# Performance work log

Hardware: AMD Instinct MI355X
Metric: run time of the kernel (lower is better)

Reference implementation:

```python
import jax, jax.numpy as jnp
import numpy as np

ALPHA = 0.2      # LeakyReLU negative slope
NEG = -9e15     # mask fill value, as in pyGAT

B, N, NFEAT, NHID, NCLASS, NHEADS = 4, 2048, 128, 64, 32, 8


def setup_inputs() -> dict:
    key = jax.random.key(0)
    ks = jax.random.split(key, 8)
    x = jax.random.normal(ks[0], (B, N, NFEAT), dtype=jnp.float32)
    adj = jax.random.randint(ks[1], (B, N, N), 0, 2, dtype=jnp.int32)
    W = jax.random.normal(ks[2], (NHEADS, NFEAT, NHID), dtype=jnp.float32) * 0.1
    a1 = jax.random.normal(ks[3], (NHEADS, NHID), dtype=jnp.float32) * 0.1
    a2 = jax.random.normal(ks[4], (NHEADS, NHID), dtype=jnp.float32) * 0.1
    Wo = jax.random.normal(ks[5], (NHEADS * NHID, NCLASS), dtype=jnp.float32) * 0.1
    ao1 = jax.random.normal(ks[6], (NCLASS,), dtype=jnp.float32) * 0.1
    ao2 = jax.random.normal(ks[7], (NCLASS,), dtype=jnp.float32) * 0.1
    return {"x": x, "adj": adj, "W": W, "a1": a1, "a2": a2,
            "Wo": Wo, "ao1": ao1, "ao2": ao2}


def _gat_forward(x, adj, W, a1, a2, Wo, ao1, ao2):
    mask = adj > 0  # [B, N, N]
    # --- multi-head layer (concat=True) ---
    Wh = jnp.einsum('bnf,hfd->bhnd', x, W)          # [B,H,N,nhid]
    f1 = jnp.einsum('bhnd,hd->bhn', Wh, a1)          # Wh @ a[:nhid]
    f2 = jnp.einsum('bhnd,hd->bhn', Wh, a2)          # Wh @ a[nhid:]
    e = jax.nn.leaky_relu(f1[..., :, None] + f2[..., None, :], ALPHA)
    att = jax.nn.softmax(jnp.where(mask[:, None], e, NEG), axis=-1)
    h = jax.nn.elu(jnp.einsum('bhnm,bhmd->bhnd', att, Wh))  # [B,H,N,nhid]
    # torch.cat along dim=2: [B, N, H*nhid]
    h = jnp.transpose(h, (0, 2, 1, 3)).reshape(B, N, NHEADS * NHID)
    # (dropout layers are no-ops in eval mode)
    # --- output head (concat=False, no ELU) ---
    Wh2 = jnp.einsum('bnf,fc->bnc', h, Wo)           # [B,N,nclass]
    g1 = jnp.einsum('bnc,c->bn', Wh2, ao1)
    g2 = jnp.einsum('bnc,c->bn', Wh2, ao2)
    e2 = jax.nn.leaky_relu(g1[:, :, None] + g2[:, None, :], ALPHA)
    att2 = jax.nn.softmax(jnp.where(mask, e2, NEG), axis=-1)
    return jnp.einsum('bnm,bmc->bnc', att2, Wh2)     # [B,N,nclass]


def reference(x, adj, W, a1, a2, Wo, ao1, ao2):
    return _gat_forward(x, adj, W, a1, a2, Wo, ao1, ao2)
```

## Files before the change

kernel.cpp:

```cpp
#include <hip/hip_runtime.h>


typedef short  short8  __attribute__((ext_vector_type(8)));
typedef float  float4_ __attribute__((ext_vector_type(4)));
typedef float  float2_ __attribute__((ext_vector_type(2)));
typedef unsigned int uint4_ __attribute__((ext_vector_type(4)));

#if __has_builtin(__builtin_amdgcn_exp2f)
#define EXP2(x) __builtin_amdgcn_exp2f(x)
#else
#define EXP2(x) __expf((x) * 0.69314718055994531f)
#endif
#define LOG2E 1.44269504088896340f

static __device__ __forceinline__ unsigned short f2bf(float f) {
  unsigned u = __float_as_uint(f);
  u += 0x7fffu + ((u >> 16) & 1u);
  return (unsigned short)(u >> 16);
}
static __device__ __forceinline__ unsigned pk2bf(float a, float b) {
  return (unsigned)f2bf(a) | ((unsigned)f2bf(b) << 16);
}

static __device__ __forceinline__ unsigned bitm(unsigned mb, int jj) {
#if __has_builtin(__builtin_amdgcn_sbfe)
  return (unsigned)__builtin_amdgcn_sbfe((int)mb, jj, 1);
#else
  return 0u - ((mb >> jj) & 1u);
#endif
}

static __device__ __forceinline__ unsigned wpair(float2_ t, unsigned m0, unsigned m1) {
  float2_ l = __builtin_elementwise_max(t * 0.2f, t);
  unsigned e0 = __float_as_uint(EXP2(l.x)) & m0;
  unsigned e1 = __float_as_uint(EXP2(l.y)) & m1;
  return __builtin_amdgcn_perm(e1, e0, 0x07060302u);
}

__global__ __launch_bounds__(256) void k_wfrag(
    const float* __restrict__ Wm, short* __restrict__ Wf) {
  const int T = blockIdx.x * 256 + threadIdx.x;
  const int lane = T & 63;
  int r = T >> 6;
  const int nt = r & 3; r >>= 2;
  const int kstep = r & 3; r >>= 2;
  const int h = r;
  const int kk = kstep * 32 + (lane >> 4) * 8;
  const int n = nt * 16 + (lane & 15);
  const float* sp = Wm + h * 8192 + kk * 64 + n;
  short8 o;
  #pragma unroll
  for (int jj = 0; jj < 8; ++jj) o[jj] = (short)f2bf(sp[jj * 64]);
  *(short8*)(Wf + T * 8) = o;
}

__global__ __launch_bounds__(256) void k_front(
    const int* __restrict__ adj, unsigned long long* __restrict__ maskb,
    const float* __restrict__ x, const short* __restrict__ Wf,
    const float* __restrict__ a1, const float* __restrict__ a2,
    short* __restrict__ WhF, float* __restrict__ f1, float* __restrict__ f2) {
  __shared__ float wsm[64 * 68];
  const int bx = blockIdx.x;
  const int t = threadIdx.x;
  if (bx >= 1024) {
    const int lane = t & 63, wid = t >> 6;
    const int s = lane & 15;
    const long long row0 = (long long)(bx - 1024) * 4;
    for (int rr = 0; rr < 4; ++rr) {
      const long long row = row0 + rr;
      const int4* src = (const int4*)(adj + row * 2048);
      #pragma unroll
      for (int c = 0; c < 2; ++c) {
        int4 v = src[c * 256 + t];
        unsigned nib = (v.x != 0 ? 1u : 0u) | (v.y != 0 ? 2u : 0u) |
                       (v.z != 0 ? 4u : 0u) | (v.w != 0 ? 8u : 0u);
        unsigned lo = (s < 8) ? (nib << (s * 4)) : 0u;
        unsigned hi = (s >= 8) ? (nib << ((s - 8) * 4)) : 0u;
        #pragma unroll
        for (int off = 1; off < 16; off <<= 1) {
          lo |= __shfl_xor(lo, off);
          hi |= __shfl_xor(hi, off);
        }
        if (s == 0) {
          int word = c * 16 + wid * 4 + (lane >> 4);
          maskb[row * 32 + word] = ((unsigned long long)hi << 32) | (unsigned long long)lo;
        }
      }
    }
    return;
  }
  const int itile = bx & 31, bh = bx >> 5;
  const int b = bh >> 3, h = bh & 7;
  const int i0 = itile * 64;
  const int lane = t & 63, w = t >> 6;
  const int cl = lane & 15, q = lane >> 4;
  const float* xrow = x + ((long long)b * 2048 + i0 + w * 16 + cl) * 128;
  const short* wfh = Wf + h * 8192;
  float4_ acc0 = {0.f, 0.f, 0.f, 0.f}, acc1 = acc0, acc2 = acc0, acc3 = acc0;
  #pragma unroll
  for (int kstep = 0; kstep < 4; ++kstep) {
    const float* xp = xrow + kstep * 32 + q * 8;
    const float4 xa = *(const float4*)xp;
    const float4 xb = *(const float4*)(xp + 4);
    uint4_ ap;
    ap.x = pk2bf(xa.x, xa.y);
    ap.y = pk2bf(xa.z, xa.w);
    ap.z = pk2bf(xb.x, xb.y);
    ap.w = pk2bf(xb.z, xb.w);
    const short8 af = __builtin_bit_cast(short8, ap);
    const short* bp = wfh + kstep * 2048 + lane * 8;
    const short8 b0 = *(const short8*)(bp);
    const short8 b1 = *(const short8*)(bp + 512);
    const short8 b2 = *(const short8*)(bp + 1024);
    const short8 b3 = *(const short8*)(bp + 1536);
    acc0 = __builtin_amdgcn_mfma_f32_16x16x32_bf16(af, b0, acc0, 0, 0, 0);
    acc1 = __builtin_amdgcn_mfma_f32_16x16x32_bf16(af, b1, acc1, 0, 0, 0);
    acc2 = __builtin_amdgcn_mfma_f32_16x16x32_bf16(af, b2, acc2, 0, 0, 0);
    acc3 = __builtin_amdgcn_mfma_f32_16x16x32_bf16(af, b3, acc3, 0, 0, 0);
  }
  {
    float4_ accs[4] = {acc0, acc1, acc2, acc3};
    #pragma unroll
    for (int nt = 0; nt < 4; ++nt)
      #pragma unroll
      for (int reg = 0; reg < 4; ++reg)
        wsm[(w * 16 + q * 4 + reg) * 68 + nt * 16 + cl] = accs[nt][reg];
  }
  __syncthreads();
  {
    const int row = t >> 2, seg = t & 3;
    const float* wr = wsm + row * 68 + seg * 16;
    const float4* a1p = (const float4*)(a1 + h * 64 + seg * 16);
    const float4* a2p = (const float4*)(a2 + h * 64 + seg * 16);
    float p1 = 0.f, p2 = 0.f;
    #pragma unroll
    for (int u = 0; u < 4; ++u) {
      const float4 wv = *(const float4*)(wr + u * 4);
      const float4 v1 = a1p[u];
      const float4 v2 = a2p[u];
      p1 += wv.x * v1.x + wv.y * v1.y + wv.z * v1.z + wv.w * v1.w;
      p2 += wv.x * v2.x + wv.y * v2.y + wv.z * v2.z + wv.w * v2.w;
    }
    p1 += __shfl_xor(p1, 1); p1 += __shfl_xor(p1, 2);
    p2 += __shfl_xor(p2, 1); p2 += __shfl_xor(p2, 2);
    if (seg == 0) {
      f1[(long long)bh * 2048 + i0 + row] = p1 * LOG2E;
      f2[(long long)bh * 2048 + i0 + row] = p2 * LOG2E;
    }
  }
  #pragma unroll
  for (int u = 0; u < 2; ++u) {
    const int idx = u * 256 + t;
    const int l2 = idx & 63, nt2 = (idx >> 6) & 3, ks2 = idx >> 8;
    const int jrow = ks2 * 32 + (l2 >> 4) * 8;
    const int d = nt2 * 16 + (l2 & 15);
    short8 o;
    #pragma unroll
    for (int jj = 0; jj < 8; ++jj) o[jj] = (short)f2bf(wsm[(jrow + jj) * 68 + d]);
    const long long off = (long long)bh * 131072 + (long long)itile * 4096 +
                          ks2 * 2048 + nt2 * 512 + l2 * 8;
    *(short8*)(WhF + off) = o;
  }
}

__global__ __launch_bounds__(256) void k_attn1(
    const short* __restrict__ whf, const float* __restrict__ f1v,
    const float* __restrict__ f2v, const unsigned long long* __restrict__ maskb,
    float* __restrict__ h1) {
  __shared__ short bsm[2][8192];
  __shared__ float f2s[2048];
  const int bh = blockIdx.y, b = bh >> 3, hh = bh & 7;
  const int t = threadIdx.x;
  const int lane = t & 63, wid = t >> 6;
  const int cl = lane & 15, q = lane >> 4;
  const long long i_g = (long long)blockIdx.x * 64 + wid * 16 + cl;
  const float f1i = f1v[(long long)bh * 2048 + i_g];
  const float2_ f1i2 = {f1i, f1i};
  const uint2* mpp = (const uint2*)(maskb + ((long long)b * 2048 + i_g) * 32);
  const float* f2b = f2v + (long long)bh * 2048;
  const short* whfb = whf + (long long)bh * 131072;
  const float4* gB = (const float4*)whfb;
  const short8 vones = {16256, 16256, 16256, 16256, 16256, 16256, 16256, 16256};
  ((float4*)f2s)[t] = ((const float4*)f2b)[t];
  ((float4*)f2s)[256 + t] = ((const float4*)f2b)[256 + t];
  {
    float4 st0[4];
    #pragma unroll
    for (int u = 0; u < 4; ++u) st0[u] = gB[u * 256 + t];
    #pragma unroll
    for (int u = 0; u < 4; ++u) ((float4*)bsm[0])[u * 256 + t] = st0[u];
  }
  uint2 mw0_c = mpp[0], mw1_c = mpp[1];
  float4_ acc0 = {0.f, 0.f, 0.f, 0.f}, acc1 = acc0, acc2 = acc0, acc3 = acc0;
  float4_ accz = acc0;
  const int qs = q * 8;
  for (int s = 0; s < 16; ++s) {
    float4 stn0, stn1, stn2, stn3;
    if (s < 15) {
      const float4* gp = gB + (s + 1) * 1024 + t;
      stn0 = gp[0]; stn1 = gp[256]; stn2 = gp[512]; stn3 = gp[768];
    }
    const uint2 mwA = mw0_c, mwB = mw1_c;
    if (s < 15) { mw0_c = mpp[s * 2 + 2]; mw1_c = mpp[s * 2 + 3]; }
    __syncthreads();
    const short* bsb = bsm[s & 1] + lane * 8;
    #pragma unroll
    for (int jc2 = 0; jc2 < 2; ++jc2) {
      const int jc = s * 2 + jc2;
      const uint2 mw = jc2 ? mwB : mwA;
      #pragma unroll
      for (int ks = 0; ks < 2; ++ks) {
        const unsigned mb = (ks ? mw.y : mw.x) >> qs;
        const float* fp = f2s + jc * 64 + ks * 32 + qs;
        const float4 fa = *(const float4*)fp;
        const float4 fb = *(const float4*)(fp + 4);
        uint4_ pk;
        pk.x = wpair(f1i2 + (float2_){fa.x, fa.y}, bitm(mb, 0), bitm(mb, 1));
        pk.y = wpair(f1i2 + (float2_){fa.z, fa.w}, bitm(mb, 2), bitm(mb, 3));
        pk.z = wpair(f1i2 + (float2_){fb.x, fb.y}, bitm(mb, 4), bitm(mb, 5));
        pk.w = wpair(f1i2 + (float2_){fb.z, fb.w}, bitm(mb, 6), bitm(mb, 7));
        const short8 af = __builtin_bit_cast(short8, pk);
        const short* bp = bsb + (jc2 * 2 + ks) * 2048;
        short8 b0 = *(const short8*)(bp);
        short8 b1 = *(const short8*)(bp + 512);
        short8 b2 = *(const short8*)(bp + 1024);
        short8 b3 = *(const short8*)(bp + 1536);
        acc0 = __builtin_amdgcn_mfma_f32_16x16x32_bf16(af, b0, acc0, 0, 0, 0);
        acc1 = __builtin_amdgcn_mfma_f32_16x16x32_bf16(af, b1, acc1, 0, 0, 0);
        acc2 = __builtin_amdgcn_mfma_f32_16x16x32_bf16(af, b2, acc2, 0, 0, 0);
        acc3 = __builtin_amdgcn_mfma_f32_16x16x32_bf16(af, b3, acc3, 0, 0, 0);
        accz = __builtin_amdgcn_mfma_f32_16x16x32_bf16(af, vones, accz, 0, 0, 0);
      }
    }
    if (s < 15) {
      float4* dp = (float4*)bsm[(s + 1) & 1] + t;
      dp[0] = stn0; dp[256] = stn1; dp[512] = stn2; dp[768] = stn3;
    }
  }
  float4_ accs[4] = {acc0, acc1, acc2, acc3};
  #pragma unroll
  for (int reg = 0; reg < 4; ++reg) {
    const int ir = q * 4 + reg;
    const float rz = 1.f / accz[reg];
    const long long row = (long long)blockIdx.x * 64 + wid * 16 + ir;
    float* op = h1 + ((long long)b * 2048 + row) * 512 + hh * 64 + cl;
    #pragma unroll
    for (int nt = 0; nt < 4; ++nt) {
      float v = accs[nt][reg] * rz;
      v = (v > 0.f) ? v : (__expf(v) - 1.f);
      op[nt * 16] = v;
    }
  }
}

__global__ __launch_bounds__(256) void k_ogemm(
    const float* __restrict__ h1, const float* __restrict__ Wo,
    const float* __restrict__ ao1, const float* __restrict__ ao2,
    short* __restrict__ Wh2F, float* __restrict__ g1, float* __restrict__ g2) {
  __shared__ float hsm[32 * 512];
  __shared__ float w2s[32 * 33];
  const long long r0 = (long long)blockIdx.x * 32;
  const int t = threadIdx.x;
  const int c = t & 31, ty = t >> 5;
  const float4* src = (const float4*)(h1 + r0 * 512);
  float4* dstv = (float4*)hsm;
  #pragma unroll
  for (int j = 0; j < 16; ++j) dstv[j * 256 + t] = src[j * 256 + t];
  __syncthreads();
  float acc0 = 0.f, acc1 = 0.f, acc2 = 0.f, acc3 = 0.f;
  for (int kc = 0; kc < 128; ++kc) {
    const int k = kc * 4;
    const float w0 = Wo[(k + 0) * 32 + c];
    const float w1 = Wo[(k + 1) * 32 + c];
    const float w2 = Wo[(k + 2) * 32 + c];
    const float w3 = Wo[(k + 3) * 32 + c];
    const float4 ha = *(const float4*)&hsm[(ty + 0) * 512 + k];
    const float4 hb = *(const float4*)&hsm[(ty + 8) * 512 + k];
    const float4 hc = *(const float4*)&hsm[(ty + 16) * 512 + k];
    const float4 hd = *(const float4*)&hsm[(ty + 24) * 512 + k];
    acc0 += ha.x * w0 + ha.y * w1 + ha.z * w2 + ha.w * w3;
    acc1 += hb.x * w0 + hb.y * w1 + hb.z * w2 + hb.w * w3;
    acc2 += hc.x * w0 + hc.y * w1 + hc.z * w2 + hc.w * w3;
    acc3 += hd.x * w0 + hd.y * w1 + hd.z * w2 + hd.w * w3;
  }
  const float a1c = ao1[c], a2c = ao2[c];
  const float accs[4] = {acc0, acc1, acc2, acc3};
  #pragma unroll
  for (int m = 0; m < 4; ++m) {
    const long long row = r0 + ty + 8 * m;
    w2s[(ty + 8 * m) * 33 + c] = accs[m];
    float p1 = accs[m] * a1c, p2 = accs[m] * a2c;
    #pragma unroll
    for (int off = 1; off < 32; off <<= 1) {
      p1 += __shfl_xor(p1, off);
      p2 += __shfl_xor(p2, off);
    }
    if (c == 0) { g1[row] = p1 * LOG2E; g2[row] = p2 * LOG2E; }
  }
  __syncthreads();
  if (t < 128) {
    const int l2 = t & 63, nt2 = t >> 6;
    const int g = blockIdx.x >> 6, jc = (blockIdx.x >> 1) & 31, ks2 = blockIdx.x & 1;
    const int lr = (l2 >> 4) * 8;
    const int d = nt2 * 16 + (l2 & 15);
    short8 o;
    #pragma unroll
    for (int jj = 0; jj < 8; ++jj) o[jj] = (short)f2bf(w2s[(lr + jj) * 33 + d]);
    const long long off = (long long)g * 65536 + jc * 2048 + ks2 * 1024 +
                          nt2 * 512 + l2 * 8;
    *(short8*)(Wh2F + off) = o;
  }
}

__global__ __launch_bounds__(256) void k_attn2(
    const short* __restrict__ whf2, const float* __restrict__ g1v,
    const float* __restrict__ g2v, const unsigned long long* __restrict__ maskb,
    float* __restrict__ outp) {
  __shared__ float accs[4][16][33];
  __shared__ float zsh[64];
  const int b = blockIdx.y;
  const long long i0 = (long long)blockIdx.x * 16;
  const int t = threadIdx.x, lane = t & 63, wid = t >> 6;
  const int cl = lane & 15, q = lane >> 4;
  const float g1i = g1v[(long long)b * 2048 + i0 + cl];
  const float2_ g1i2 = {g1i, g1i};
  const uint2* mpp = (const uint2*)(maskb + ((long long)b * 2048 + i0 + cl) * 32);
  const float* g2b = g2v + (long long)b * 2048;
  const short* wb = whf2 + (long long)b * 65536;
  const short8 vones = {16256, 16256, 16256, 16256, 16256, 16256, 16256, 16256};
  float4_ acc0 = {0.f, 0.f, 0.f, 0.f}, acc1 = acc0, accz = acc0;
  const int qs = q * 8;
  const int jc0 = wid * 8;
  uint2 mw_c = mpp[jc0];
  float4 fa0_c = *(const float4*)(g2b + jc0 * 64 + qs);
  float4 fb0_c = *(const float4*)(g2b + jc0 * 64 + qs + 4);
  float4 fa1_c = *(const float4*)(g2b + jc0 * 64 + 32 + qs);
  float4 fb1_c = *(const float4*)(g2b + jc0 * 64 + 36 + qs);
  for (int c8 = 0; c8 < 8; ++c8) {
    const int jc = jc0 + c8;
    const uint2 mw = mw_c;
    const float4 fa0 = fa0_c, fb0 = fb0_c, fa1 = fa1_c, fb1 = fb1_c;
    {
      const int jn = jc + ((c8 < 7) ? 1 : 0);
      const float* fp = g2b + jn * 64 + qs;
      mw_c = mpp[jn];
      fa0_c = *(const float4*)fp;
      fb0_c = *(const float4*)(fp + 4);
      fa1_c = *(const float4*)(fp + 32);
      fb1_c = *(const float4*)(fp + 36);
    }
    const short* bb = wb + (jc * 2) * 1024 + lane * 8;
    {
      const unsigned mb = mw.x >> qs;
      uint4_ pk;
      pk.x = wpair(g1i2 + (float2_){fa0.x, fa0.y}, bitm(mb, 0), bitm(mb, 1));
      pk.y = wpair(g1i2 + (float2_){fa0.z, fa0.w}, bitm(mb, 2), bitm(mb, 3));
      pk.z = wpair(g1i2 + (float2_){fb0.x, fb0.y}, bitm(mb, 4), bitm(mb, 5));
      pk.w = wpair(g1i2 + (float2_){fb0.z, fb0.w}, bitm(mb, 6), bitm(mb, 7));
      const short8 af = __builtin_bit_cast(short8, pk);
      short8 b0 = *(const short8*)bb;
      short8 b1 = *(const short8*)(bb + 512);
      acc0 = __builtin_amdgcn_mfma_f32_16x16x32_bf16(af, b0, acc0, 0, 0, 0);
      acc1 = __builtin_amdgcn_mfma_f32_16x16x32_bf16(af, b1, acc1, 0, 0, 0);
      accz = __builtin_amdgcn_mfma_f32_16x16x32_bf16(af, vones, accz, 0, 0, 0);
    }
    {
      const unsigned mb = mw.y >> qs;
      uint4_ pk;
      pk.x = wpair(g1i2 + (float2_){fa1.x, fa1.y}, bitm(mb, 0), bitm(mb, 1));
      pk.y = wpair(g1i2 + (float2_){fa1.z, fa1.w}, bitm(mb, 2), bitm(mb, 3));
      pk.z = wpair(g1i2 + (float2_){fb1.x, fb1.y}, bitm(mb, 4), bitm(mb, 5));
      pk.w = wpair(g1i2 + (float2_){fb1.z, fb1.w}, bitm(mb, 6), bitm(mb, 7));
      const short8 af = __builtin_bit_cast(short8, pk);
      const short* bk = bb + 1024;
      short8 b0 = *(const short8*)bk;
      short8 b1 = *(const short8*)(bk + 512);
      acc0 = __builtin_amdgcn_mfma_f32_16x16x32_bf16(af, b0, acc0, 0, 0, 0);
      acc1 = __builtin_amdgcn_mfma_f32_16x16x32_bf16(af, b1, acc1, 0, 0, 0);
      accz = __builtin_amdgcn_mfma_f32_16x16x32_bf16(af, vones, accz, 0, 0, 0);
    }
  }
  if (cl == 0) {
    #pragma unroll
    for (int reg = 0; reg < 4; ++reg) zsh[wid * 16 + q * 4 + reg] = accz[reg];
  }
  float4_ a01[2] = {acc0, acc1};
  #pragma unroll
  for (int nt = 0; nt < 2; ++nt)
    #pragma unroll
    for (int reg = 0; reg < 4; ++reg)
      accs[wid][q * 4 + reg][nt * 16 + cl] = a01[nt][reg];
  __syncthreads();
  #pragma unroll
  for (int r = 0; r < 2; ++r) {
    int o = r * 256 + t;
    int il = o >> 5, c = o & 31;
    float s = accs[0][il][c] + accs[1][il][c] + accs[2][il][c] + accs[3][il][c];
    float Z = zsh[il] + zsh[16 + il] + zsh[32 + il] + zsh[48 + il];
    outp[((long long)b * 2048 + i0 + il) * 32 + c] = s / Z;
  }
}

extern "C" void kernel_launch(void* const* d_in, const int* in_sizes, int n_in,
                              void* d_out, int out_size, void* d_ws, size_t ws_size,
                              hipStream_t stream) {
  const float* x   = (const float*)d_in[0];
  const int*   adj = (const int*)d_in[1];
  const float* W   = (const float*)d_in[2];
  const float* a1  = (const float*)d_in[3];
  const float* a2  = (const float*)d_in[4];
  const float* Wo  = (const float*)d_in[5];
  const float* ao1 = (const float*)d_in[6];
  const float* ao2 = (const float*)d_in[7];
  float* out = (float*)d_out;
  char* ws = (char*)d_ws;

  unsigned long long* maskb = (unsigned long long*)(ws + 0);
  short* Wf   = (short*)(ws + 2097152);
  short* WhF  = (short*)(ws + 18874368);
  float* f1   = (float*)(ws + 27262976);
  float* f2   = (float*)(ws + 27525120);
  float* h1   = (float*)(ws + 27787264);
  short* Wh2F = (short*)(ws + 45613056);
  float* g1   = (float*)(ws + 46137344);
  float* g2   = (float*)(ws + 46170112);

  hipLaunchKernelGGL(k_wfrag, dim3(32), dim3(256), 0, stream, W, Wf);
  hipLaunchKernelGGL(k_front, dim3(3072), dim3(256), 0, stream, adj, maskb,
                     x, Wf, a1, a2, WhF, f1, f2);
  hipLaunchKernelGGL(k_attn1, dim3(32, 32), dim3(256), 0, stream, WhF, f1, f2, maskb, h1);
  hipLaunchKernelGGL(k_ogemm, dim3(256), dim3(256), 0, stream, h1, Wo, ao1, ao2,
                     Wh2F, g1, g2);
  hipLaunchKernelGGL(k_attn2, dim3(128, 4), dim3(256), 0, stream, Wh2F, g1, g2, maskb, out);
}
```

Measured before the change: 190.6 us.

## Factor attention exponentials into per-row and per-column terms; MFMA output GEMM

The per-element exp2(leaky_relu(f1+f2)) is rewritten as max(exp2(f1)*exp2(f2), exp2(0.2f1)*exp2(0.2f2)). The per-column exponentials are precomputed once and packed as two bf16 values, so the inner attention loop does two multiplies and a max instead of exp2 calls. The first attention kernel now writes h in bf16 MFMA fragment layout, and the output GEMM becomes an MFMA kernel using a pre-fragmented Wo. Exp-based factorization can overflow or underflow for large logits, and bf16 rounding of the exponentials reduces accuracy.

```diff
diff --git a/kernel.cpp b/kernel.cpp
--- a/kernel.cpp
+++ b/kernel.cpp
@@ -21,6 +21,9 @@
 static __device__ __forceinline__ unsigned pk2bf(float a, float b) {
   return (unsigned)f2bf(a) | ((unsigned)f2bf(b) << 16);
 }
+static __device__ __forceinline__ unsigned upack(float s) {
+  return ((unsigned)f2bf(EXP2(0.2f * s)) << 16) | f2bf(EXP2(s));
+}
 
 static __device__ __forceinline__ unsigned bitm(unsigned mb, int jj) {
 #if __has_builtin(__builtin_amdgcn_sbfe)
@@ -30,35 +33,53 @@
 #endif
 }
 
-static __device__ __forceinline__ unsigned wpair(float2_ t, unsigned m0, unsigned m1) {
-  float2_ l = __builtin_elementwise_max(t * 0.2f, t);
-  unsigned e0 = __float_as_uint(EXP2(l.x)) & m0;
-  unsigned e1 = __float_as_uint(EXP2(l.y)) & m1;
+static __device__ __forceinline__ unsigned wmax2(unsigned w0, unsigned w1,
+    unsigned m0, unsigned m1, float2_ Av, float2_ A2v) {
+  float2_ lo = {__uint_as_float(w0 << 16), __uint_as_float(w1 << 16)};
+  float2_ hi = {__uint_as_float(w0 & 0xFFFF0000u), __uint_as_float(w1 & 0xFFFF0000u)};
+  float2_ p = Av * lo;
+  float2_ n = A2v * hi;
+  float2_ m = __builtin_elementwise_max(p, n);
+  unsigned e0 = __float_as_uint(m.x) & m0;
+  unsigned e1 = __float_as_uint(m.y) & m1;
   return __builtin_amdgcn_perm(e1, e0, 0x07060302u);
 }
 
 __global__ __launch_bounds__(256) void k_wfrag(
-    const float* __restrict__ Wm, short* __restrict__ Wf) {
-  const int T = blockIdx.x * 256 + threadIdx.x;
-  const int lane = T & 63;
-  int r = T >> 6;
-  const int nt = r & 3; r >>= 2;
-  const int kstep = r & 3; r >>= 2;
-  const int h = r;
-  const int kk = kstep * 32 + (lane >> 4) * 8;
-  const int n = nt * 16 + (lane & 15);
-  const float* sp = Wm + h * 8192 + kk * 64 + n;
-  short8 o;
-  #pragma unroll
-  for (int jj = 0; jj < 8; ++jj) o[jj] = (short)f2bf(sp[jj * 64]);
-  *(short8*)(Wf + T * 8) = o;
+    const float* __restrict__ Wm, const float* __restrict__ Wo,
+    short* __restrict__ Wf, short* __restrict__ WoF) {
+  if (blockIdx.x < 32) {
+    const int T = blockIdx.x * 256 + threadIdx.x;
+    const int lane = T & 63;
+    int r = T >> 6;
+    const int nt = r & 3; r >>= 2;
+    const int kstep = r & 3; r >>= 2;
+    const int h = r;
+    const int kk = kstep * 32 + (lane >> 4) * 8;
+    const int n = nt * 16 + (lane & 15);
+    const float* sp = Wm + h * 8192 + kk * 64 + n;
+    short8 o;
+    #pragma unroll
+    for (int jj = 0; jj < 8; ++jj) o[jj] = (short)f2bf(sp[jj * 64]);
+    *(short8*)(Wf + T * 8) = o;
+  } else {
+    const int T = (blockIdx.x - 32) * 256 + threadIdx.x;
+    const int lane = T & 63;
+    const int nt = (T >> 6) & 1, kstep = T >> 7;
+    const int kk = kstep * 32 + (lane >> 4) * 8;
+    const int n = nt * 16 + (lane & 15);
+    short8 o;
+    #pragma unroll
+    for (int jj = 0; jj < 8; ++jj) o[jj] = (short)f2bf(Wo[(kk + jj) * 32 + n]);
+    *(short8*)(WoF + T * 8) = o;
+  }
 }
 
 __global__ __launch_bounds__(256) void k_front(
     const int* __restrict__ adj, unsigned long long* __restrict__ maskb,
     const float* __restrict__ x, const short* __restrict__ Wf,
     const float* __restrict__ a1, const float* __restrict__ a2,
-    short* __restrict__ WhF, float* __restrict__ f1, float* __restrict__ f2) {
+    short* __restrict__ WhF, float* __restrict__ f1, unsigned* __restrict__ f2p) {
   __shared__ float wsm[64 * 68];
   const int bx = blockIdx.x;
   const int t = threadIdx.x;
@@ -145,7 +166,7 @@
     p2 += __shfl_xor(p2, 1); p2 += __shfl_xor(p2, 2);
     if (seg == 0) {
       f1[(long long)bh * 2048 + i0 + row] = p1 * LOG2E;
-      f2[(long long)bh * 2048 + i0 + row] = p2 * LOG2E;
+      f2p[(long long)bh * 2048 + i0 + row] = upack(p2 * LOG2E);
     }
   }
   #pragma unroll
@@ -165,24 +186,25 @@
 
 __global__ __launch_bounds__(256) void k_attn1(
     const short* __restrict__ whf, const float* __restrict__ f1v,
-    const float* __restrict__ f2v, const unsigned long long* __restrict__ maskb,
-    float* __restrict__ h1) {
+    const unsigned* __restrict__ f2pv, const unsigned long long* __restrict__ maskb,
+    short* __restrict__ hA) {
   __shared__ short bsm[2][8192];
-  __shared__ float f2s[2048];
+  __shared__ unsigned f2s[2048];
   const int bh = blockIdx.y, b = bh >> 3, hh = bh & 7;
   const int t = threadIdx.x;
   const int lane = t & 63, wid = t >> 6;
   const int cl = lane & 15, q = lane >> 4;
   const long long i_g = (long long)blockIdx.x * 64 + wid * 16 + cl;
   const float f1i = f1v[(long long)bh * 2048 + i_g];
-  const float2_ f1i2 = {f1i, f1i};
+  const float A = EXP2(f1i), A2 = EXP2(0.2f * f1i);
+  const float2_ Av = {A, A}, A2v = {A2, A2};
   const uint2* mpp = (const uint2*)(maskb + ((long long)b * 2048 + i_g) * 32);
-  const float* f2b = f2v + (long long)bh * 2048;
+  const unsigned* f2b = f2pv + (long long)bh * 2048;
   const short* whfb = whf + (long long)bh * 131072;
   const float4* gB = (const float4*)whfb;
   const short8 vones = {16256, 16256, 16256, 16256, 16256, 16256, 16256, 16256};
-  ((float4*)f2s)[t] = ((const float4*)f2b)[t];
-  ((float4*)f2s)[256 + t] = ((const float4*)f2b)[256 + t];
+  ((uint4_*)f2s)[t] = ((const uint4_*)f2b)[t];
+  ((uint4_*)f2s)[256 + t] = ((const uint4_*)f2b)[256 + t];
   {
     float4 st0[4];
     #pragma unroll
@@ -211,14 +233,14 @@
       #pragma unroll
       for (int ks = 0; ks < 2; ++ks) {
         const unsigned mb = (ks ? mw.y : mw.x) >> qs;
-        const float* fp = f2s + jc * 64 + ks * 32 + qs;
-        const float4 fa = *(const float4*)fp;
-        const float4 fb = *(const float4*)(fp + 4);
+        const unsigned* up = f2s + jc * 64 + ks * 32 + qs;
+        const uint4_ wa = *(const uint4_*)up;
+        const uint4_ wb = *(const uint4_*)(up + 4);
         uint4_ pk;
-        pk.x = wpair(f1i2 + (float2_){fa.x, fa.y}, bitm(mb, 0), bitm(mb, 1));
-        pk.y = wpair(f1i2 + (float2_){fa.z, fa.w}, bitm(mb, 2), bitm(mb, 3));
-        pk.z = wpair(f1i2 + (float2_){fb.x, fb.y}, bitm(mb, 4), bitm(mb, 5));
-        pk.w = wpair(f1i2 + (float2_){fb.z, fb.w}, bitm(mb, 6), bitm(mb, 7));
+        pk.x = wmax2(wa.x, wa.y, bitm(mb, 0), bitm(mb, 1), Av, A2v);
+        pk.y = wmax2(wa.z, wa.w, bitm(mb, 2), bitm(mb, 3), Av, A2v);
+        pk.z = wmax2(wb.x, wb.y, bitm(mb, 4), bitm(mb, 5), Av, A2v);
+        pk.w = wmax2(wb.z, wb.w, bitm(mb, 6), bitm(mb, 7), Av, A2v);
         const short8 af = __builtin_bit_cast(short8, pk);
         const short* bp = bsb + (jc2 * 2 + ks) * 2048;
         short8 b0 = *(const short8*)(bp);
@@ -237,75 +259,87 @@
       dp[0] = stn0; dp[256] = stn1; dp[512] = stn2; dp[768] = stn3;
     }
   }
-  float4_ accs[4] = {acc0, acc1, acc2, acc3};
+  __syncthreads();
+  float* hs = (float*)bsm;
+  {
+    float4_ accs[4] = {acc0, acc1, acc2, acc3};
+    #pragma unroll
+    for (int reg = 0; reg < 4; ++reg) {
+      const float rz = 1.f / accz[reg];
+      #pragma unroll
+      for (int nt = 0; nt < 4; ++nt) {
+        float v = accs[nt][reg] * rz;
+        v = (v > 0.f) ? v : (__expf(v) - 1.f);
+        hs[(wid * 16 + q * 4 + reg) * 68 + nt * 16 + cl] = v;
+      }
+    }
+  }
+  __syncthreads();
+  const int rtg0 = b * 128 + blockIdx.x * 4;
+  #pragma unroll
+  for (int u = 0; u < 2; ++u) {
+    const int id = u * 256 + t;
+    const int l2 = id & 63, ks2 = (id >> 6) & 1, rtile = id >> 7;
+    const int rowl = rtile * 16 + (l2 & 15);
+    const int d = ks2 * 32 + (l2 >> 4) * 8;
+    const float* hp = hs + rowl * 68 + d;
+    const float4 va = *(const float4*)hp;
+    const float4 vb = *(const float4*)(hp + 4);
+    uint4_ o;
+    o.x = pk2bf(va.x, va.y); o.y = pk2bf(va.z, va.w);
+    o.z = pk2bf(vb.x, vb.y); o.w = pk2bf(vb.z, vb.w);
+    const long long rt = rtg0 + rtile;
+    const int kstep = hh * 2 + ks2;
+    *(uint4_*)(hA + ((rt * 16 + kstep) * 64 + l2) * 8) = o;
+  }
+}
+
+__global__ __launch_bounds__(128) void k_ogemm(
+    const short* __restrict__ hA, const short* __restrict__ WoF,
+    const float* __restrict__ ao1, const float* __restrict__ ao2,
+    short* __restrict__ Wh2F, float* __restrict__ g1, unsigned* __restrict__ g2p) {
+  __shared__ float w2s[32 * 36];
+  const int t = threadIdx.x, lane = t & 63, wv = t >> 6;
+  const int cl = lane & 15, q = lane >> 4;
+  const long long rt = (long long)blockIdx.x * 2 + wv;
+  float4_ acc0 = {0.f, 0.f, 0.f, 0.f}, acc1 = acc0;
+  const short* ap = hA + rt * 8192 + lane * 8;
+  const short* bp = WoF + lane * 8;
+  #pragma unroll
+  for (int kstep = 0; kstep < 16; ++kstep) {
+    const short8 af = *(const short8*)(ap + kstep * 512);
+    const short8 b0 = *(const short8*)(bp + kstep * 1024);
+    const short8 b1 = *(const short8*)(bp + kstep * 1024 + 512);
+    acc0 = __builtin_amdgcn_mfma_f32_16x16x32_bf16(af, b0, acc0, 0, 0, 0);
+    acc1 = __builtin_amdgcn_mfma_f32_16x16x32_bf16(af, b1, acc1, 0, 0, 0);
+  }
+  const float o1a = ao1[cl], o1b = ao1[cl + 16];
+  const float o2a = ao2[cl], o2b = ao2[cl + 16];
   #pragma unroll
   for (int reg = 0; reg < 4; ++reg) {
-    const int ir = q * 4 + reg;
-    const float rz = 1.f / accz[reg];
-    const long long row = (long long)blockIdx.x * 64 + wid * 16 + ir;
-    float* op = h1 + ((long long)b * 2048 + row) * 512 + hh * 64 + cl;
-    #pragma unroll
-    for (int nt = 0; nt < 4; ++nt) {
-      float v = accs[nt][reg] * rz;
-      v = (v > 0.f) ? v : (__expf(v) - 1.f);
-      op[nt * 16] = v;
-    }
-  }
-}
-
-__global__ __launch_bounds__(256) void k_ogemm(
-    const float* __restrict__ h1, const float* __restrict__ Wo,
-    const float* __restrict__ ao1, const float* __restrict__ ao2,
-    short* __restrict__ Wh2F, float* __restrict__ g1, float* __restrict__ g2) {
-  __shared__ float hsm[32 * 512];
-  __shared__ float w2s[32 * 33];
-  const long long r0 = (long long)blockIdx.x * 32;
-  const int t = threadIdx.x;
-  const int c = t & 31, ty = t >> 5;
-  const float4* src = (const float4*)(h1 + r0 * 512);
-  float4* dstv = (float4*)hsm;
-  #pragma unroll
-  for (int j = 0; j < 16; ++j) dstv[j * 256 + t] = src[j * 256 + t];
+    const int rowl = wv * 16 + q * 4 + reg;
+    w2s[rowl * 36 + cl] = acc0[reg];
+    w2s[rowl * 36 + 16 + cl] = acc1[reg];
+    float p1 = acc0[reg] * o1a + acc1[reg] * o1b;
+    float p2 = acc0[reg] * o2a + acc1[reg] * o2b;
+    p1 += __shfl_xor(p1, 1); p1 += __shfl_xor(p1, 2);
+    p1 += __shfl_xor(p1, 4); p1 += __shfl_xor(p1, 8);
+    p2 += __shfl_xor(p2, 1); p2 += __shfl_xor(p2, 2);
+    p2 += __shfl_xor(p2, 4); p2 += __shfl_xor(p2, 8);
+    if (cl == 0) {
+      const long long row = (long long)blockIdx.x * 32 + rowl;
+      g1[row] = p1 * LOG2E;
+      g2p[row] = upack(p2 * LOG2E);
+    }
+  }
   __syncthreads();
-  float acc0 = 0.f, acc1 = 0.f, acc2 = 0.f, acc3 = 0.f;
-  for (int kc = 0; kc < 128; ++kc) {
-    const int k = kc * 4;
-    const float w0 = Wo[(k + 0) * 32 + c];
-    const float w1 = Wo[(k + 1) * 32 + c];
-    const float w2 = Wo[(k + 2) * 32 + c];
-    const float w3 = Wo[(k + 3) * 32 + c];
-    const float4 ha = *(const float4*)&hsm[(ty + 0) * 512 + k];
-    const float4 hb = *(const float4*)&hsm[(ty + 8) * 512 + k];
-    const float4 hc = *(const float4*)&hsm[(ty + 16) * 512 + k];
-    const float4 hd = *(const float4*)&hsm[(ty + 24) * 512 + k];
-    acc0 += ha.x * w0 + ha.y * w1 + ha.z * w2 + ha.w * w3;
-    acc1 += hb.x * w0 + hb.y * w1 + hb.z * w2 + hb.w * w3;
-    acc2 += hc.x * w0 + hc.y * w1 + hc.z * w2 + hc.w * w3;
-    acc3 += hd.x * w0 + hd.y * w1 + hd.z * w2 + hd.w * w3;
-  }
-  const float a1c = ao1[c], a2c = ao2[c];
-  const float accs[4] = {acc0, acc1, acc2, acc3};
-  #pragma unroll
-  for (int m = 0; m < 4; ++m) {
-    const long long row = r0 + ty + 8 * m;
-    w2s[(ty + 8 * m) * 33 + c] = accs[m];
-    float p1 = accs[m] * a1c, p2 = accs[m] * a2c;
-    #pragma unroll
-    for (int off = 1; off < 32; off <<= 1) {
-      p1 += __shfl_xor(p1, off);
-      p2 += __shfl_xor(p2, off);
-    }
-    if (c == 0) { g1[row] = p1 * LOG2E; g2[row] = p2 * LOG2E; }
-  }
-  __syncthreads();
-  if (t < 128) {
+  {
     const int l2 = t & 63, nt2 = t >> 6;
     const int g = blockIdx.x >> 6, jc = (blockIdx.x >> 1) & 31, ks2 = blockIdx.x & 1;
-    const int lr = (l2 >> 4) * 8;
-    const int d = nt2 * 16 + (l2 & 15);
+    const int kb = (l2 >> 4) * 8, n = nt2 * 16 + (l2 & 15);
     short8 o;
     #pragma unroll
-    for (int jj = 0; jj < 8; ++jj) o[jj] = (short)f2bf(w2s[(lr + jj) * 33 + d]);
+    for (int jj = 0; jj < 8; ++jj) o[jj] = (short)f2bf(w2s[(kb + jj) * 36 + n]);
     const long long off = (long long)g * 65536 + jc * 2048 + ks2 * 1024 +
                           nt2 * 512 + l2 * 8;
     *(short8*)(Wh2F + off) = o;
@@ -314,7 +348,7 @@
 
 __global__ __launch_bounds__(256) void k_attn2(
     const short* __restrict__ whf2, const float* __restrict__ g1v,
-    const float* __restrict__ g2v, const unsigned long long* __restrict__ maskb,
+    const unsigned* __restrict__ g2pv, const unsigned long long* __restrict__ maskb,
     float* __restrict__ outp) {
   __shared__ float accs[4][16][33];
   __shared__ float zsh[64];
@@ -323,40 +357,41 @@
   const int t = threadIdx.x, lane = t & 63, wid = t >> 6;
   const int cl = lane & 15, q = lane >> 4;
   const float g1i = g1v[(long long)b * 2048 + i0 + cl];
-  const float2_ g1i2 = {g1i, g1i};
+  const float A = EXP2(g1i), A2 = EXP2(0.2f * g1i);
+  const float2_ Av = {A, A}, A2v = {A2, A2};
   const uint2* mpp = (const uint2*)(maskb + ((long long)b * 2048 + i0 + cl) * 32);
-  const float* g2b = g2v + (long long)b * 2048;
+  const unsigned* g2b = g2pv + (long long)b * 2048;
   const short* wb = whf2 + (long long)b * 65536;
   const short8 vones = {16256, 16256, 16256, 16256, 16256, 16256, 16256, 16256};
   float4_ acc0 = {0.f, 0.f, 0.f, 0.f}, acc1 = acc0, accz = acc0;
   const int qs = q * 8;
   const int jc0 = wid * 8;
   uint2 mw_c = mpp[jc0];
-  float4 fa0_c = *(const float4*)(g2b + jc0 * 64 + qs);
-  float4 fb0_c = *(const float4*)(g2b + jc0 * 64 + qs + 4);
-  float4 fa1_c = *(const float4*)(g2b + jc0 * 64 + 32 + qs);
-  float4 fb1_c = *(const float4*)(g2b + jc0 * 64 + 36 + qs);
+  uint4_ wa0_c = *(const uint4_*)(g2b + jc0 * 64 + qs);
+  uint4_ wb0_c = *(const uint4_*)(g2b + jc0 * 64 + qs + 4);
+  uint4_ wa1_c = *(const uint4_*)(g2b + jc0 * 64 + 32 + qs);
+  uint4_ wb1_c = *(const uint4_*)(g2b + jc0 * 64 + 36 + qs);
   for (int c8 = 0; c8 < 8; ++c8) {
     const int jc = jc0 + c8;
     const uint2 mw = mw_c;
-    const float4 fa0 = fa0_c, fb0 = fb0_c, fa1 = fa1_c, fb1 = fb1_c;
+    const uint4_ wa0 = wa0_c, wb0 = wb0_c, wa1 = wa1_c, wb1 = wb1_c;
     {
       const int jn = jc + ((c8 < 7) ? 1 : 0);
-      const float* fp = g2b + jn * 64 + qs;
+      const unsigned* fp = g2b + jn * 64 + qs;
       mw_c = mpp[jn];
-      fa0_c = *(const float4*)fp;
-      fb0_c = *(const float4*)(fp + 4);
-      fa1_c = *(const float4*)(fp + 32);
-      fb1_c = *(const float4*)(fp + 36);
+      wa0_c = *(const uint4_*)fp;
+      wb0_c = *(const uint4_*)(fp + 4);
+      wa1_c = *(const uint4_*)(fp + 32);
+      wb1_c = *(const uint4_*)(fp + 36);
     }
     const short* bb = wb + (jc * 2) * 1024 + lane * 8;
     {
       const unsigned mb = mw.x >> qs;
       uint4_ pk;
-      pk.x = wpair(g1i2 + (float2_){fa0.x, fa0.y}, bitm(mb, 0), bitm(mb, 1));
-      pk.y = wpair(g1i2 + (float2_){fa0.z, fa0.w}, bitm(mb, 2), bitm(mb, 3));
-      pk.z = wpair(g1i2 + (float2_){fb0.x, fb0.y}, bitm(mb, 4), bitm(mb, 5));
-      pk.w = wpair(g1i2 + (float2_){fb0.z, fb0.w}, bitm(mb, 6), bitm(mb, 7));
+      pk.x = wmax2(wa0.x, wa0.y, bitm(mb, 0), bitm(mb, 1), Av, A2v);
+      pk.y = wmax2(wa0.z, wa0.w, bitm(mb, 2), bitm(mb, 3), Av, A2v);
+      pk.z = wmax2(wb0.x, wb0.y, bitm(mb, 4), bitm(mb, 5), Av, A2v);
+      pk.w = wmax2(wb0.z, wb0.w, bitm(mb, 6), bitm(mb, 7), Av, A2v);
       const short8 af = __builtin_bit_cast(short8, pk);
       short8 b0 = *(const short8*)bb;
       short8 b1 = *(const short8*)(bb + 512);
@@ -367,10 +402,10 @@
     {
       const unsigned mb = mw.y >> qs;
       uint4_ pk;
-      pk.x = wpair(g1i2 + (float2_){fa1.x, fa1.y}, bitm(mb, 0), bitm(mb, 1));
-      pk.y = wpair(g1i2 + (float2_){fa1.z, fa1.w}, bitm(mb, 2), bitm(mb, 3));
-      pk.z = wpair(g1i2 + (float2_){fb1.x, fb1.y}, bitm(mb, 4), bitm(mb, 5));
-      pk.w = wpair(g1i2 + (float2_){fb1.z, fb1.w}, bitm(mb, 6), bitm(mb, 7));
+      pk.x = wmax2(wa1.x, wa1.y, bitm(mb, 0), bitm(mb, 1), Av, A2v);
+      pk.y = wmax2(wa1.z, wa1.w, bitm(mb, 2), bitm(mb, 3), Av, A2v);
+      pk.z = wmax2(wb1.x, wb1.y, bitm(mb, 4), bitm(mb, 5), Av, A2v);
+      pk.w = wmax2(wb1.z, wb1.w, bitm(mb, 6), bitm(mb, 7), Av, A2v);
       const short8 af = __builtin_bit_cast(short8, pk);
       const short* bk = bb + 1024;
       short8 b0 = *(const short8*)bk;
@@ -417,19 +452,20 @@
 
   unsigned long long* maskb = (unsigned long long*)(ws + 0);
   short* Wf   = (short*)(ws + 2097152);
+  short* WoF  = (short*)(ws + 2228224);
   short* WhF  = (short*)(ws + 18874368);
   float* f1   = (float*)(ws + 27262976);
-  float* f2   = (float*)(ws + 27525120);
-  float* h1   = (float*)(ws + 27787264);
+  unsigned* f2p = (unsigned*)(ws + 27525120);
+  short* hA   = (short*)(ws + 27787264);
   short* Wh2F = (short*)(ws + 45613056);
   float* g1   = (float*)(ws + 46137344);
-  float* g2   = (float*)(ws + 46170112);
-
-  hipLaunchKernelGGL(k_wfrag, dim3(32), dim3(256), 0, stream, W, Wf);
+  unsigned* g2p = (unsigned*)(ws + 46170112);
+
+  hipLaunchKernelGGL(k_wfrag, dim3(40), dim3(256), 0, stream, W, Wo, Wf, WoF);
   hipLaunchKernelGGL(k_front, dim3(3072), dim3(256), 0, stream, adj, maskb,
-                     x, Wf, a1, a2, WhF, f1, f2);
-  hipLaunchKernelGGL(k_attn1, dim3(32, 32), dim3(256), 0, stream, WhF, f1, f2, maskb, h1);
-  hipLaunchKernelGGL(k_ogemm, dim3(256), dim3(256), 0, stream, h1, Wo, ao1, ao2,
-                     Wh2F, g1, g2);
-  hipLaunchKernelGGL(k_attn2, dim3(128, 4), dim3(256), 0, stream, Wh2F, g1, g2, maskb, out);
-}
+                     x, Wf, a1, a2, WhF, f1, f2p);
+  hipLaunchKernelGGL(k_attn1, dim3(32, 32), dim3(256), 0, stream, WhF, f1, f2p, maskb, hA);
+  hipLaunchKernelGGL(k_ogemm, dim3(256), dim3(128), 0, stream, hA, WoF, ao1, ao2,
+                     Wh2F, g1, g2p);
+  hipLaunchKernelGGL(k_attn2, dim3(128, 4), dim3(256), 0, stream, Wh2F, g1, g2p, maskb, out);
+}
```

Result: faster. 181.0 us (-5.1%).
